# Kernel optimization log

Hardware: AMD Instinct MI355X
Metric: run time of the kernel (lower is better)

The kernel has to match this reference:

```python
import jax, jax.numpy as jnp
import numpy as np

NEG_SLOPE = 0.2

def setup_inputs() -> dict:
    key = jax.random.key(0)
    k1, k2, k3, k4 = jax.random.split(key, 4)
    B, n, d_in, d_out = 8, 2048, 128, 128
    x = jax.random.normal(k1, (B, n, d_in), dtype=jnp.float32)
    adj = jax.random.uniform(k2, (B, n, n), dtype=jnp.float32)
    # glorot init for W: std = sqrt(2/(fan_in+fan_out))
    W = jax.random.normal(k3, (d_in, d_out), dtype=jnp.float32) * np.sqrt(2.0 / (d_in + d_out))
    a = jax.random.normal(k4, (2 * d_out,), dtype=jnp.float32) * np.sqrt(2.0 / (2 * d_out + 1))
    return {"x": x, "adj": adj, "W": W, "a": a}

def reference(x, adj, W, a):
    d_out = W.shape[1]
    h = jnp.einsum('bni,io->bno', x, W)               # [B,n,d_out]
    x_weighted = jnp.einsum('bnm,bmo->bno', adj, h)   # adj @ Wx
    # additive attention: a @ concat(h_i, h_j) == h_i@a_src + h_j@a_dst
    a_src, a_dst = a[:d_out], a[d_out:]
    s_i = h @ a_src                                   # [B,n]
    s_j = h @ a_dst                                   # [B,n]
    e = jax.nn.leaky_relu(s_i[:, :, None] + s_j[:, None, :], NEG_SLOPE)  # [B,n,n]
    alpha = jax.nn.softmax(e, axis=2)
    out = jnp.einsum('bnm,bmo->bno', alpha, h) + x_weighted
    return jax.nn.leaky_relu(out, NEG_SLOPE)
```

## Files before the change

### kernel.cpp

```cpp
#include <hip/hip_runtime.h>
#include <hip/hip_bf16.h>

#define NEG 0.2f
#define LOG2E 1.4426950408889634f

typedef __attribute__((ext_vector_type(8))) short bf16x8;
typedef __attribute__((ext_vector_type(4))) float f32x4;
typedef __attribute__((ext_vector_type(4))) int int4v;

__device__ __forceinline__ float lrelu(float t){ return fmaxf(t, NEG * t); }
__device__ __forceinline__ float fast_exp2(float x){
  float r; asm("v_exp_f32 %0, %1" : "=v"(r) : "v"(x)); return r;
}
__device__ __forceinline__ unsigned short f2bf(float f){
  union { float f; unsigned int u; } v; v.f = f;
  unsigned int r = v.u + 0x7FFFu + ((v.u >> 16) & 1u);
  return (unsigned short)(r >> 16);
}

__global__ __launch_bounds__(256) void k0_wt(const float* __restrict__ W,
                                             unsigned short* __restrict__ Wt){
  __shared__ __align__(16) unsigned short wl[128*136];
  const int t = threadIdx.x;
  {
    const int k = t >> 1, oh = (t & 1) * 64;
#pragma unroll 8
    for (int e = 0; e < 64; ++e)
      wl[(oh + e)*136 + k] = f2bf(W[k*128 + oh + e]);
  }
  __syncthreads();
  {
    const int o = t >> 1, ks = (t & 1) * 64;
#pragma unroll
    for (int g = 0; g < 8; ++g){
      int4v v = *(const int4v*)(wl + o*136 + ks + g*8);
      *(int4v*)(Wt + o*128 + ks + g*8) = v;
    }
  }
}

__global__ __launch_bounds__(256) void k1_fused(const float* __restrict__ x,
                                                const unsigned short* __restrict__ Wt,
                                                const float* __restrict__ a,
                                                unsigned short* __restrict__ ht,
                                                float* __restrict__ ssrcL,
                                                float* __restrict__ sdstL){
  __shared__ __align__(16) unsigned short wtl[128*136];
  __shared__ __align__(16) unsigned short xl[32*136];
  __shared__ __align__(16) unsigned short tlw[128*34];
  __shared__ float sred[2][4][2][16];
  const int t = threadIdx.x;
  const int bx = blockIdx.x;
  const int b  = bx >> 6;
  const int jt = bx & 63;
  const long rowbase = (long)bx * 32;
  {
    const int o = t >> 1, seg = (t & 1) * 64;
    const int4v* src = (const int4v*)(Wt + o*128 + seg);
    int4v* dst = (int4v*)(wtl + o*136 + seg);
#pragma unroll
    for (int g = 0; g < 8; ++g) dst[g] = src[g];
  }
  {
    const int i = t >> 3, ks = (t & 7) * 16;
    const f32x4* src = (const f32x4*)(x + (rowbase + i)*128 + ks);
    unsigned int q[8];
#pragma unroll
    for (int g = 0; g < 4; ++g){
      f32x4 v = src[g];
      q[g*2]   = (unsigned)f2bf(v[0]) | ((unsigned)f2bf(v[1]) << 16);
      q[g*2+1] = (unsigned)f2bf(v[2]) | ((unsigned)f2bf(v[3]) << 16);
    }
    int4v* dst = (int4v*)(xl + i*136 + ks);
    dst[0] = *(int4v*)&q[0];
    dst[1] = *(int4v*)&q[4];
  }
  __syncthreads();
  const int w = t >> 6, lane = t & 63, lr = lane & 15, hi = lane >> 4;
  f32x4 zro = {0.f, 0.f, 0.f, 0.f};
  f32x4 acc00 = zro, acc01 = zro, acc10 = zro, acc11 = zro;
#pragma unroll
  for (int ks = 0; ks < 4; ++ks){
    const bf16x8 a0 = *(const bf16x8*)(wtl + (w*32      + lr)*136 + ks*32 + hi*8);
    const bf16x8 a1 = *(const bf16x8*)(wtl + (w*32 + 16 + lr)*136 + ks*32 + hi*8);
    const bf16x8 b0 = *(const bf16x8*)(xl + (     lr)*136 + ks*32 + hi*8);
    const bf16x8 b1 = *(const bf16x8*)(xl + (16 + lr)*136 + ks*32 + hi*8);
    acc00 = __builtin_amdgcn_mfma_f32_16x16x32_bf16(a0, b0, acc00, 0, 0, 0);
    acc01 = __builtin_amdgcn_mfma_f32_16x16x32_bf16(a0, b1, acc01, 0, 0, 0);
    acc10 = __builtin_amdgcn_mfma_f32_16x16x32_bf16(a1, b0, acc10, 0, 0, 0);
    acc11 = __builtin_amdgcn_mfma_f32_16x16x32_bf16(a1, b1, acc11, 0, 0, 0);
  }
  {
    const f32x4 as0 = *(const f32x4*)(a +       w*32      + hi*4);
    const f32x4 as1 = *(const f32x4*)(a +       w*32 + 16 + hi*4);
    const f32x4 ad0 = *(const f32x4*)(a + 128 + w*32      + hi*4);
    const f32x4 ad1 = *(const f32x4*)(a + 128 + w*32 + 16 + hi*4);
    float ps0, ps1, pd0, pd1;
    {
      f32x4 u = acc00*as0 + acc10*as1;  ps0 = u[0]+u[1]+u[2]+u[3];
      f32x4 v = acc01*as0 + acc11*as1;  ps1 = v[0]+v[1]+v[2]+v[3];
      f32x4 p = acc00*ad0 + acc10*ad1;  pd0 = p[0]+p[1]+p[2]+p[3];
      f32x4 r = acc01*ad0 + acc11*ad1;  pd1 = r[0]+r[1]+r[2]+r[3];
    }
#pragma unroll
    for (int off = 16; off <= 32; off <<= 1){
      ps0 += __shfl_xor(ps0, off); ps1 += __shfl_xor(ps1, off);
      pd0 += __shfl_xor(pd0, off); pd1 += __shfl_xor(pd1, off);
    }
    if (hi == 0){
      sred[0][w][0][lr] = ps0; sred[0][w][1][lr] = ps1;
      sred[1][w][0][lr] = pd0; sred[1][w][1][lr] = pd1;
    }
  }
#pragma unroll
  for (int q = 0; q < 4; ++q){
    tlw[(w*32      + hi*4 + q)*34      + lr] = f2bf(acc00[q]);
    tlw[(w*32      + hi*4 + q)*34 + 16 + lr] = f2bf(acc01[q]);
    tlw[(w*32 + 16 + hi*4 + q)*34      + lr] = f2bf(acc10[q]);
    tlw[(w*32 + 16 + hi*4 + q)*34 + 16 + lr] = f2bf(acc11[q]);
  }
  __syncthreads();
  {
    const int o = t >> 1, jseg = (t & 1) * 16;
    const unsigned int* src = (const unsigned int*)(tlw + o*34 + jseg);
    unsigned int p[8];
#pragma unroll
    for (int g = 0; g < 8; ++g) p[g] = src[g];
    unsigned short* dst = ht + (long)b*262144 + (long)o*2048 + jt*32 + jseg;
    ((int4v*)dst)[0] = *(int4v*)&p[0];
    ((int4v*)dst)[1] = *(int4v*)&p[4];
  }
  if (t < 64){
    const int sel = t >> 5, jl = t & 31;
    const int ig = jl >> 4, l2 = jl & 15;
    const float s = sred[sel][0][ig][l2] + sred[sel][1][ig][l2]
                  + sred[sel][2][ig][l2] + sred[sel][3][ig][l2];
    if (sel == 0) ssrcL[rowbase + jl] = s * LOG2E;
    else          sdstL[rowbase + jl] = s * LOG2E;
  }
}

__global__ __launch_bounds__(256) void k2_ml(const float* __restrict__ ssrcL,
                                             const float* __restrict__ sdstL,
                                             float* __restrict__ carr){
  const int lane = threadIdx.x & 63;
  const long row = (long)blockIdx.x * 4 + (threadIdx.x >> 6);
  const int b = (int)(row >> 11);
  const float siL = ssrcL[row];
  const float* sd = sdstL + (long)b*2048;
  float mx = -3.4e38f;
#pragma unroll
  for (int k = 0; k < 8; ++k){
    f32x4 v = *(const f32x4*)(sd + lane*4 + k*256);
    mx = fmaxf(mx, fmaxf(fmaxf(v[0], v[1]), fmaxf(v[2], v[3])));
  }
#pragma unroll
  for (int off = 1; off <= 32; off <<= 1) mx = fmaxf(mx, __shfl_xor(mx, off));
  const float mL = lrelu(siL + mx);
  float sum = 0.f;
#pragma unroll
  for (int k = 0; k < 8; ++k){
    f32x4 v = *(const f32x4*)(sd + lane*4 + k*256);
#pragma unroll
    for (int e = 0; e < 4; ++e) sum += fast_exp2(lrelu(siL + v[e]) - mL);
  }
#pragma unroll
  for (int off = 1; off <= 32; off <<= 1) sum += __shfl_xor(sum, off);
  if (lane == 0) carr[row] = mL + __log2f(sum);
}

__global__ __launch_bounds__(256) void k3_main(const float* __restrict__ adj,
                                               const unsigned short* __restrict__ ht,
                                               const float* __restrict__ ssrcL,
                                               const float* __restrict__ sdstL,
                                               const float* __restrict__ carr,
                                               float* __restrict__ out){
  __shared__ __align__(16) char smem[40960];
  unsigned short* tl = (unsigned short*)smem;
  float* red = (float*)smem;
  const int t   = threadIdx.x;
  const int bx  = blockIdx.x;
  const int b   = bx >> 6;
  const int i0  = (bx & 63) * 32;
  const int lane = t & 63;
  const int lr  = lane & 15, hi = lane >> 4;
  const int kh  = t >> 7, wr = (t >> 6) & 1;
  const int rowi = i0 + wr*16 + lr;
  const long rowg = (long)b*2048 + rowi;
  const float siL = ssrcL[rowg];
  const float Ci  = carr[rowg];
  const float* adjrow = adj + rowg*2048 + kh*1024 + hi*8;
  const float* sdb    = sdstL + (long)b*2048 + kh*1024 + hi*8;
  const unsigned short* htg = ht + (long)b*262144;
  const int so = t >> 2, sseg = t & 3;
  const unsigned short* sgp0 = htg + (long)so*2048 + sseg*8;
  const unsigned short* sgp1 = htg + (long)(so + 64)*2048 + sseg*8;
  const int woff0 = so*40 + sseg*8;
  const int woff1 = (so + 64)*40 + sseg*8;

  f32x4 zro = {0.f, 0.f, 0.f, 0.f};
  f32x4 acc[8];
#pragma unroll
  for (int i = 0; i < 8; ++i) acc[i] = zro;

  *(int4v*)(tl + 0*5120 + woff0) = *(const int4v*)(sgp0);
  *(int4v*)(tl + 1*5120 + woff0) = *(const int4v*)(sgp0 + 1024);
  *(int4v*)(tl + 0*5120 + woff1) = *(const int4v*)(sgp1);
  *(int4v*)(tl + 1*5120 + woff1) = *(const int4v*)(sgp1 + 1024);
  int4v pA0 = *(const int4v*)(sgp0 + 32);
  int4v pA1 = *(const int4v*)(sgp0 + 1024 + 32);
  int4v pA2 = *(const int4v*)(sgp1 + 32);
  int4v pA3 = *(const int4v*)(sgp1 + 1024 + 32);
  int4v pB0 = *(const int4v*)(sgp0 + 64);
  int4v pB1 = *(const int4v*)(sgp0 + 1024 + 64);
  int4v pB2 = *(const int4v*)(sgp1 + 64);
  int4v pB3 = *(const int4v*)(sgp1 + 1024 + 64);
  f32x4 aA0 = *(const f32x4*)(adjrow);
  f32x4 aA1 = *(const f32x4*)(adjrow + 4);
  f32x4 dA0 = *(const f32x4*)(sdb);
  f32x4 dA1 = *(const f32x4*)(sdb + 4);
  f32x4 aB0 = *(const f32x4*)(adjrow + 32);
  f32x4 aB1 = *(const f32x4*)(adjrow + 36);
  f32x4 dB0 = *(const f32x4*)(sdb + 32);
  f32x4 dB1 = *(const f32x4*)(sdb + 36);
  asm volatile("s_waitcnt lgkmcnt(0)" ::: "memory");
  __builtin_amdgcn_s_barrier();
  __builtin_amdgcn_sched_barrier(0);

#define K3_ITER(KT, P0, P1, P2, P3, A0, A1, D0, D1, BW, BR)  do{                 \
    *(int4v*)(tl + ((BW)*2+0)*5120 + woff0) = P0;           \
    *(int4v*)(tl + ((BW)*2+1)*5120 + woff0) = P1;                                \
    *(int4v*)(tl + ((BW)*2+0)*5120 + woff1) = P2;                                \
    *(int4v*)(tl + ((BW)*2+1)*5120 + woff1) = P3;                                \
    {  const int jo3 = ((KT)+3 < 32 ? (KT)+3 : 31)*32;      \
       P0 = *(const int4v*)(sgp0 + jo3);                                         \
       P1 = *(const int4v*)(sgp0 + 1024 + jo3);                                  \
       P2 = *(const int4v*)(sgp1 + jo3);                                         \
       P3 = *(const int4v*)(sgp1 + 1024 + jo3); }                                \
    bf16x8 af;                                                                   \
    {  float w[8];                                                               \
       _Pragma("unroll")                                                         \
       for (int e = 0; e < 4; ++e){                                              \
         const float u0 = siL + D0[e];                                           \
         w[e]     = A0[e] + fast_exp2(lrelu(u0) - Ci);                           \
         const float u1 = siL + D1[e];                                           \
         w[4 + e] = A1[e] + fast_exp2(lrelu(u1) - Ci);                           \
       }                                                                         \
       const unsigned int p01 = __builtin_amdgcn_perm(__float_as_uint(w[1]), __float_as_uint(w[0]), 0x07060302u); \
       const unsigned int p23 = __builtin_amdgcn_perm(__float_as_uint(w[3]), __float_as_uint(w[2]), 0x07060302u); \
       const unsigned int p45 = __builtin_amdgcn_perm(__float_as_uint(w[5]), __float_as_uint(w[4]), 0x07060302u); \
       const unsigned int p67 = __builtin_amdgcn_perm(__float_as_uint(w[7]), __float_as_uint(w[6]), 0x07060302u); \
       int4v ai = {(int)p01, (int)p23, (int)p45, (int)p67};                      \
       af = *(bf16x8*)&ai;                                                       \
    }                                                                            \
    {  const int jn = ((KT)+2 < 32 ? (KT)+2 : 31)*32;       \
       A0 = *(const f32x4*)(adjrow + jn);                                        \
       A1 = *(const f32x4*)(adjrow + jn + 4);                                    \
       D0 = *(const f32x4*)(sdb + jn);                                           \
       D1 = *(const f32x4*)(sdb + jn + 4); }                                     \
    __builtin_amdgcn_s_setprio(1);                                               \
    _Pragma("unroll")                                                            \
    for (int cg = 0; cg < 8; ++cg){                                              \
      const bf16x8 bfv = *(const bf16x8*)(tl + ((BR)*2+kh)*5120 + (cg*16 + lr)*40 + hi*8); \
      acc[cg] = __builtin_amdgcn_mfma_f32_16x16x32_bf16(af, bfv, acc[cg], 0, 0, 0); \
    }                                                                            \
    __builtin_amdgcn_s_setprio(0);                                               \
    asm volatile("s_waitcnt lgkmcnt(0)" ::: "memory");                           \
    __builtin_amdgcn_s_barrier();                                                \
    __builtin_amdgcn_sched_barrier(0);                                           \
  }while(0)

  for (int kt = 0; kt < 32; kt += 2){
    K3_ITER(kt,     pA0, pA1, pA2, pA3, aA0, aA1, dA0, dA1, 1, 0);
    K3_ITER(kt + 1, pB0, pB1, pB2, pB3, aB0, aB1, dB0, dB1, 0, 1);
  }
#undef K3_ITER

  if (kh == 1){
#pragma unroll
    for (int cg = 0; cg < 8; ++cg)
#pragma unroll
      for (int q = 0; q < 4; ++q)
        red[(wr*16 + hi*4 + q)*128 + cg*16 + lr] = acc[cg][q];
  }
  __syncthreads();
  if (kh == 0){
#pragma unroll
    for (int cg = 0; cg < 8; ++cg){
#pragma unroll
      for (int q = 0; q < 4; ++q){
        const int rl2 = wr*16 + hi*4 + q;
        const float v = acc[cg][q] + red[rl2*128 + cg*16 + lr];
        out[((long)b*2048 + i0 + rl2)*128 + cg*16 + lr] = lrelu(v);
      }
    }
  }
}

extern "C" void kernel_launch(void* const* d_in, const int* in_sizes, int n_in,
                              void* d_out, int out_size, void* d_ws, size_t ws_size,
                              hipStream_t stream){
  const float* x   = (const float*)d_in[0];
  const float* adj = (const float*)d_in[1];
  const float* W   = (const float*)d_in[2];
  const float* a   = (const float*)d_in[3];
  float* out = (float*)d_out;
  char* ws = (char*)d_ws;

  unsigned short* ht    = (unsigned short*)(ws);
  float*          ssrcL = (float*)(ws + 4194304);
  float*          sdstL = (float*)(ws + 4259840);
  float*          carr  = (float*)(ws + 4325376);
  unsigned short* Wt    = (unsigned short*)(ws + 4390912);

  k0_wt   <<<1,    256, 0, stream>>>(W, Wt);
  k1_fused<<<512,  256, 0, stream>>>(x, Wt, a, ht, ssrcL, sdstL);
  k2_ml   <<<4096, 256, 0, stream>>>(ssrcL, sdstL, carr);
  k3_main <<<512,  256, 0, stream>>>(adj, ht, ssrcL, sdstL, carr, out);
}
```

Baseline: 64.76 us.

## Deepen adj prefetch to four tiles, swizzle block order, set min two blocks/CU

The main attention-aggregation kernel now prefetches the adjacency and s_dst fragments four k-tiles ahead instead of two, using four register sets and a loop unrolled by four. Block indices are remapped so that consecutive blocks land on different batches. The launch bounds request two blocks per CU, which caps register use. The aim is to hide more HBM latency on the streaming adj reads, at the cost of extra registers that may spill or lower occupancy.

```diff
diff --git a/kernel.cpp b/kernel.cpp
--- a/kernel.cpp
+++ b/kernel.cpp
@@ -169,17 +169,18 @@
   if (lane == 0) carr[row] = mL + __log2f(sum);
 }
 
-__global__ __launch_bounds__(256) void k3_main(const float* __restrict__ adj,
-                                               const unsigned short* __restrict__ ht,
-                                               const float* __restrict__ ssrcL,
-                                               const float* __restrict__ sdstL,
-                                               const float* __restrict__ carr,
-                                               float* __restrict__ out){
+__global__ __launch_bounds__(256, 2) void k3_main(const float* __restrict__ adj,
+                                                  const unsigned short* __restrict__ ht,
+                                                  const float* __restrict__ ssrcL,
+                                                  const float* __restrict__ sdstL,
+                                                  const float* __restrict__ carr,
+                                                  float* __restrict__ out){
   __shared__ __align__(16) char smem[40960];
   unsigned short* tl = (unsigned short*)smem;
   float* red = (float*)smem;
   const int t   = threadIdx.x;
-  const int bx  = blockIdx.x;
+  const int bxr = blockIdx.x;
+  const int bx  = ((bxr & 7) << 6) | (bxr >> 3);
   const int b   = bx >> 6;
   const int i0  = (bx & 63) * 32;
   const int lane = t & 63;
@@ -207,36 +208,36 @@
   *(int4v*)(tl + 1*5120 + woff0) = *(const int4v*)(sgp0 + 1024);
   *(int4v*)(tl + 0*5120 + woff1) = *(const int4v*)(sgp1);
   *(int4v*)(tl + 1*5120 + woff1) = *(const int4v*)(sgp1 + 1024);
-  int4v pA0 = *(const int4v*)(sgp0 + 32);
-  int4v pA1 = *(const int4v*)(sgp0 + 1024 + 32);
-  int4v pA2 = *(const int4v*)(sgp1 + 32);
-  int4v pA3 = *(const int4v*)(sgp1 + 1024 + 32);
-  int4v pB0 = *(const int4v*)(sgp0 + 64);
-  int4v pB1 = *(const int4v*)(sgp0 + 1024 + 64);
-  int4v pB2 = *(const int4v*)(sgp1 + 64);
-  int4v pB3 = *(const int4v*)(sgp1 + 1024 + 64);
-  f32x4 aA0 = *(const f32x4*)(adjrow);
-  f32x4 aA1 = *(const f32x4*)(adjrow + 4);
-  f32x4 dA0 = *(const f32x4*)(sdb);
-  f32x4 dA1 = *(const f32x4*)(sdb + 4);
-  f32x4 aB0 = *(const f32x4*)(adjrow + 32);
-  f32x4 aB1 = *(const f32x4*)(adjrow + 36);
-  f32x4 dB0 = *(const f32x4*)(sdb + 32);
-  f32x4 dB1 = *(const f32x4*)(sdb + 36);
+  int4v hA0 = *(const int4v*)(sgp0 + 32);
+  int4v hA1 = *(const int4v*)(sgp0 + 1024 + 32);
+  int4v hA2 = *(const int4v*)(sgp1 + 32);
+  int4v hA3 = *(const int4v*)(sgp1 + 1024 + 32);
+  int4v hB0 = *(const int4v*)(sgp0 + 64);
+  int4v hB1 = *(const int4v*)(sgp0 + 1024 + 64);
+  int4v hB2 = *(const int4v*)(sgp1 + 64);
+  int4v hB3 = *(const int4v*)(sgp1 + 1024 + 64);
+  f32x4 aA0 = *(const f32x4*)(adjrow);        f32x4 aA1 = *(const f32x4*)(adjrow + 4);
+  f32x4 dA0 = *(const f32x4*)(sdb);           f32x4 dA1 = *(const f32x4*)(sdb + 4);
+  f32x4 aB0 = *(const f32x4*)(adjrow + 32);   f32x4 aB1 = *(const f32x4*)(adjrow + 36);
+  f32x4 dB0 = *(const f32x4*)(sdb + 32);      f32x4 dB1 = *(const f32x4*)(sdb + 36);
+  f32x4 aC0 = *(const f32x4*)(adjrow + 64);   f32x4 aC1 = *(const f32x4*)(adjrow + 68);
+  f32x4 dC0 = *(const f32x4*)(sdb + 64);      f32x4 dC1 = *(const f32x4*)(sdb + 68);
+  f32x4 aD0 = *(const f32x4*)(adjrow + 96);   f32x4 aD1 = *(const f32x4*)(adjrow + 100);
+  f32x4 dD0 = *(const f32x4*)(sdb + 96);      f32x4 dD1 = *(const f32x4*)(sdb + 100);
   asm volatile("s_waitcnt lgkmcnt(0)" ::: "memory");
   __builtin_amdgcn_s_barrier();
   __builtin_amdgcn_sched_barrier(0);
 
 #define K3_ITER(KT, P0, P1, P2, P3, A0, A1, D0, D1, BW, BR)  do{                 \
-    *(int4v*)(tl + ((BW)*2+0)*5120 + woff0) = P0;           \
+    *(int4v*)(tl + ((BW)*2+0)*5120 + woff0) = P0;         \
     *(int4v*)(tl + ((BW)*2+1)*5120 + woff0) = P1;                                \
     *(int4v*)(tl + ((BW)*2+0)*5120 + woff1) = P2;                                \
     *(int4v*)(tl + ((BW)*2+1)*5120 + woff1) = P3;                                \
-    {  const int jo3 = ((KT)+3 < 32 ? (KT)+3 : 31)*32;      \
-       P0 = *(const int4v*)(sgp0 + jo3);                                         \
-       P1 = *(const int4v*)(sgp0 + 1024 + jo3);                                  \
-       P2 = *(const int4v*)(sgp1 + jo3);                                         \
-       P3 = *(const int4v*)(sgp1 + 1024 + jo3); }                                \
+    {  const int j3 = ((KT)+3 < 32 ? (KT)+3 : 31)*32;          \
+       P0 = *(const int4v*)(sgp0 + j3);                                          \
+       P1 = *(const int4v*)(sgp0 + 1024 + j3);                                   \
+       P2 = *(const int4v*)(sgp1 + j3);                                          \
+       P3 = *(const int4v*)(sgp1 + 1024 + j3); }                                 \
     bf16x8 af;                                                                   \
     {  float w[8];                                                               \
        _Pragma("unroll")                                                         \
@@ -253,11 +254,11 @@
        int4v ai = {(int)p01, (int)p23, (int)p45, (int)p67};                      \
        af = *(bf16x8*)&ai;                                                       \
     }                                                                            \
-    {  const int jn = ((KT)+2 < 32 ? (KT)+2 : 31)*32;       \
-       A0 = *(const f32x4*)(adjrow + jn);                                        \
-       A1 = *(const f32x4*)(adjrow + jn + 4);                                    \
-       D0 = *(const f32x4*)(sdb + jn);                                           \
-       D1 = *(const f32x4*)(sdb + jn + 4); }                                     \
+    {  const int j4 = ((KT)+4 < 32 ? (KT)+4 : 31)*32;      \
+       A0 = *(const f32x4*)(adjrow + j4);                                        \
+       A1 = *(const f32x4*)(adjrow + j4 + 4);                                    \
+       D0 = *(const f32x4*)(sdb + j4);                                           \
+       D1 = *(const f32x4*)(sdb + j4 + 4); }                                     \
     __builtin_amdgcn_s_setprio(1);                                               \
     _Pragma("unroll")                                                            \
     for (int cg = 0; cg < 8; ++cg){                                              \
@@ -270,9 +271,11 @@
     __builtin_amdgcn_sched_barrier(0);                                           \
   }while(0)
 
-  for (int kt = 0; kt < 32; kt += 2){
-    K3_ITER(kt,     pA0, pA1, pA2, pA3, aA0, aA1, dA0, dA1, 1, 0);
-    K3_ITER(kt + 1, pB0, pB1, pB2, pB3, aB0, aB1, dB0, dB1, 0, 1);
+  for (int kt = 0; kt < 32; kt += 4){
+    K3_ITER(kt,     hA0, hA1, hA2, hA3, aA0, aA1, dA0, dA1, 1, 0);
+    K3_ITER(kt + 1, hB0, hB1, hB2, hB3, aB0, aB1, dB0, dB1, 0, 1);
+    K3_ITER(kt + 2, hA0, hA1, hA2, hA3, aC0, aC1, dC0, dC1, 1, 0);
+    K3_ITER(kt + 3, hB0, hB1, hB2, hB3, aD0, aD1, dD0, dD1, 0, 1);
   }
 #undef K3_ITER
 
```

New measurement: 63.18 us. 2.4% less time.
